# Optimization experiments

Measured on AMD Instinct MI355X. Metric: run time of the kernel, lower is better.

The kernel has to match this reference:

```python
import jax, jax.numpy as jnp
import numpy as np

N, D, H = 4096, 256, 8
DH = D // H
E = 131072
LN_EPS = 1e-5
NEG = -1e9


def setup_inputs() -> dict:
    key = jax.random.key(0)
    ks = jax.random.split(key, 10)
    s = 0.02
    return {
        "embeddings": jax.random.normal(ks[0], (N, D), dtype=jnp.float32),
        "edge_index": jax.random.randint(ks[1], (2, E), 0, N, dtype=jnp.int64),
        "in_proj_w": jax.random.normal(ks[2], (3 * D, D), dtype=jnp.float32) * s,
        "in_proj_b": jnp.zeros((3 * D,), jnp.float32),
        "out_w": jax.random.normal(ks[3], (D, D), dtype=jnp.float32) * s,
        "out_b": jnp.zeros((D,), jnp.float32),
        "lin_w": jax.random.normal(ks[4], (D, D), dtype=jnp.float32) * s,
        "lin_b": jnp.zeros((D,), jnp.float32),
        "ln_g": jnp.ones((D,), jnp.float32),
        "ln_beta": jnp.zeros((D,), jnp.float32),
    }


def reference(embeddings, edge_index, in_proj_w, in_proj_b, out_w, out_b, lin_w, lin_b, ln_g, ln_beta):
    n, d = embeddings.shape
    src, dst = edge_index[0], edge_index[1]
    # symmetric adjacency (per-cell neighbor set = unique nodes touching the cell),
    # self excluded (matches `neighbor_indices != cell_idx`)
    adj = jnp.zeros((n, n), dtype=bool).at[src, dst].set(True).at[dst, src].set(True)
    adj = adj & ~jnp.eye(n, dtype=bool)
    has_nb = adj.any(axis=1)  # [N]

    # MultiheadAttention (eval: dropout off), single query per cell over its neighbors
    qkv = embeddings @ in_proj_w.T + in_proj_b          # [N, 3D]
    q, k, v = jnp.split(qkv, 3, axis=-1)
    qh = q.reshape(n, H, DH)
    kh = k.reshape(n, H, DH)
    vh = v.reshape(n, H, DH)
    scale = 1.0 / np.sqrt(DH).astype(np.float32)
    scores = jnp.einsum('nhd,mhd->nhm', qh, kh) * scale  # [N, H, N]
    scores = jnp.where(adj[:, None, :], scores, NEG)
    attn = jax.nn.softmax(scores, axis=-1)
    ctx = jnp.einsum('nhm,mhd->nhd', attn, vh).reshape(n, d)
    ctx = ctx @ out_w.T + out_b
    # cells with no neighbors keep their own embedding
    x = jnp.where(has_nb[:, None], ctx, embeddings)

    # context_transform: Linear -> LayerNorm -> GELU (dropout off in eval)
    y = x @ lin_w.T + lin_b
    mu = y.mean(axis=-1, keepdims=True)
    var = y.var(axis=-1, keepdims=True)
    y = (y - mu) / jnp.sqrt(var + LN_EPS) * ln_g + ln_beta
    return jax.nn.gelu(y, approximate=False)
```

## Files before the change

kernel.cpp:

```cpp
#include <hip/hip_runtime.h>
#include <math.h>

#define NN 4096
#define DD 256
#define EE 131072
#define MAXD 128
#define SP 132

typedef __attribute__((ext_vector_type(8))) short short8;
typedef __attribute__((ext_vector_type(4))) float float4v;

__device__ __forceinline__ unsigned short f2bf(float f){
    unsigned u = __float_as_uint(f);
    return (unsigned short)((u + 0x7fffu + ((u >> 16) & 1u)) >> 16);
}
__device__ __forceinline__ float blo(unsigned u){ return __uint_as_float(u << 16); }
__device__ __forceinline__ float bhi(unsigned u){ return __uint_as_float(u & 0xffff0000u); }

__device__ __forceinline__ void pack_one(const float* __restrict__ src, unsigned short* __restrict__ dst, int e){
    int lane = e & 63;
    int row = ((e >> 9) << 4) + (lane & 15);
    int k0 = ((e >> 6) & 7) * 32 + ((lane >> 4) << 3);
    const float* p = src + row * DD + k0;
    short8 v;
    #pragma unroll
    for (int j = 0; j < 8; ++j) v[j] = (short)f2bf(p[j]);
    ((short8*)dst)[e] = v;
}

__global__ void k_packw(const float* __restrict__ ipw, const float* __restrict__ ow, const float* __restrict__ lw,
                        unsigned short* __restrict__ bipw, unsigned short* __restrict__ bow,
                        unsigned short* __restrict__ blw, unsigned* __restrict__ adj){
    int e = blockIdx.x * 256 + threadIdx.x;
    for (int i = e; i < 524288; i += 40960) adj[i] = 0u;
    if (e < 24576)       pack_one(ipw, bipw, e);
    else if (e < 32768)  pack_one(ow,  bow,  e - 24576);
    else                 pack_one(lw,  blw,  e - 32768);
}

__global__ void __launch_bounds__(256) k_gqkv(const float* __restrict__ emb, const unsigned short* __restrict__ Bp,
                                              const float* __restrict__ bias, float* __restrict__ qf,
                                              unsigned short* __restrict__ kb, unsigned short* __restrict__ vb,
                                              const int* __restrict__ ei, unsigned* __restrict__ adj){
    __shared__ float sA[16 * 260];
    int bx = blockIdx.x, by = blockIdx.y;
    int t = threadIdx.x, w = t >> 6, lane = t & 63;

    int gid = (by * gridDim.x + bx) * 256 + t;
    if (gid < EE){
        int s = ei[gid], d = ei[EE + gid];
        if (s != d){
            atomicOr(&adj[s * 128 + (d >> 5)], 1u << (d & 31));
            atomicOr(&adj[d * 128 + (s >> 5)], 1u << (s & 31));
        }
    }

    #pragma unroll
    for (int i = 0; i < 16; ++i)
        sA[i * 260 + t] = emb[(bx * 16 + i) * 256 + t];
    __syncthreads();

    int arow = lane & 15, ak0 = (lane >> 4) << 3;
    short8 af[8];
    #pragma unroll
    for (int s = 0; s < 8; ++s){
        const float* p = &sA[arow * 260 + s * 32 + ak0];
        #pragma unroll
        for (int j = 0; j < 8; ++j) af[s][j] = (short)f2bf(p[j]);
    }

    const short8* B8 = (const short8*)Bp;
    float4v acc[4];
    #pragma unroll
    for (int c = 0; c < 4; ++c) acc[c] = (float4v){0.f, 0.f, 0.f, 0.f};
    #pragma unroll
    for (int s = 0; s < 8; ++s){
        #pragma unroll
        for (int c = 0; c < 4; ++c){
            int to = by * 16 + w * 4 + c;
            acc[c] = __builtin_amdgcn_mfma_f32_16x16x32_bf16(af[s], B8[(to * 8 + s) * 64 + lane], acc[c], 0, 0, 0);
        }
    }
    int q = lane >> 4, col = lane & 15;
    #pragma unroll
    for (int c = 0; c < 4; ++c){
        int o = (w * 4 + c) * 16 + col;
        float bo = bias[by * 256 + o];
        #pragma unroll
        for (int r = 0; r < 4; ++r){
            int node = bx * 16 + q * 4 + r;
            float val = acc[c][r] + bo;
            if (by == 0)      qf[node * 256 + o] = val;
            else if (by == 1) kb[node * 256 + o] = f2bf(val);
            else              vb[node * 256 + o] = f2bf(val);
        }
    }
}

__device__ __forceinline__ float dot32(const float4* qa, uint4 a, uint4 b, uint4 c, uint4 d){
    float s;
    s  = qa[0].x*blo(a.x) + qa[0].y*bhi(a.x) + qa[0].z*blo(a.y) + qa[0].w*bhi(a.y);
    s += qa[1].x*blo(a.z) + qa[1].y*bhi(a.z) + qa[1].z*blo(a.w) + qa[1].w*bhi(a.w);
    s += qa[2].x*blo(b.x) + qa[2].y*bhi(b.x) + qa[2].z*blo(b.y) + qa[2].w*bhi(b.y);
    s += qa[3].x*blo(b.z) + qa[3].y*bhi(b.z) + qa[3].z*blo(b.w) + qa[3].w*bhi(b.w);
    s += qa[4].x*blo(c.x) + qa[4].y*bhi(c.x) + qa[4].z*blo(c.y) + qa[4].w*bhi(c.y);
    s += qa[5].x*blo(c.z) + qa[5].y*bhi(c.z) + qa[5].z*blo(c.w) + qa[5].w*bhi(c.w);
    s += qa[6].x*blo(d.x) + qa[6].y*bhi(d.x) + qa[6].z*blo(d.y) + qa[6].w*bhi(d.y);
    s += qa[7].x*blo(d.z) + qa[7].y*bhi(d.z) + qa[7].z*blo(d.w) + qa[7].w*bhi(d.w);
    return s;
}

__global__ void __launch_bounds__(512) k_attn_tail(
        const float* __restrict__ qf, const unsigned short* __restrict__ kb,
        const unsigned short* __restrict__ vb, const unsigned* __restrict__ adj,
        const float* __restrict__ emb,
        const unsigned short* __restrict__ Bow, const float* __restrict__ ob,
        const unsigned short* __restrict__ Blw, const float* __restrict__ lb,
        const float* __restrict__ g, const float* __restrict__ beta,
        float* __restrict__ out){
    __shared__ float  sS[8][8][SP];
    __shared__ int    sNbr[8][MAXD];
    __shared__ short8 sPk[512];
    __shared__ float  sInv[8][8];
    __shared__ int    sDeg[8];
    int bx = blockIdx.x, t = threadIdx.x;
    int wv = t >> 6, lane = t & 63;
    int n0 = bx * 8;
    int n = n0 + wv;
    float* xs = (float*)sS;

    uint2 aw = ((const uint2*)(adj + n * 128))[lane];
    int cnt = __popc(aw.x) + __popc(aw.y);
    int pre = cnt;
    #pragma unroll
    for (int off = 1; off < 64; off <<= 1){
        int tmp = __shfl_up(pre, off);
        if (lane >= off) pre += tmp;
    }
    int tot = __shfl(pre, 63);
    int dg = (tot < MAXD) ? tot : MAXD;
    if (lane == 63) sDeg[wv] = dg;
    int base = pre - cnt;
    int mb = lane * 64;
    unsigned b0 = aw.x, b1 = aw.y;
    while (b0){ int b = __ffs(b0) - 1; b0 &= b0 - 1u; if (base < MAXD) sNbr[wv][base] = mb + b; base++; }
    mb += 32;
    while (b1){ int b = __ffs(b1) - 1; b1 &= b1 - 1u; if (base < MAXD) sNbr[wv][base] = mb + b; base++; }

    if (dg > 0){
        asm volatile("s_waitcnt lgkmcnt(0)" ::: "memory");

        int js = lane >> 3, h = lane & 7;
        float4 qa[8];
        const float4* q4 = (const float4*)(qf + n * 256 + h * 32);
        #pragma unroll
        for (int i = 0; i < 8; ++i) qa[i] = q4[i];
        for (int jb = 0; jb < dg; jb += 16){
            int j0 = jb + js, j1 = jb + 8 + js;
            bool v0 = j0 < dg, v1 = j1 < dg;
            int m0 = v0 ? sNbr[wv][j0] : sNbr[wv][0];
            int m1 = v1 ? sNbr[wv][j1] : sNbr[wv][0];
            const uint4* kr0 = (const uint4*)(kb + m0 * 256) + h * 4;
            const uint4* kr1 = (const uint4*)(kb + m1 * 256) + h * 4;
            uint4 a0 = kr0[0], a1 = kr0[1], a2 = kr0[2], a3 = kr0[3];
            uint4 c0 = kr1[0], c1 = kr1[1], c2 = kr1[2], c3 = kr1[3];
            float s0 = dot32(qa, a0, a1, a2, a3) * 0.17677669529663687f;
            float s1 = dot32(qa, c0, c1, c2, c3) * 0.17677669529663687f;
            if (v0) sS[wv][h][j0] = s0;
            if (v1) sS[wv][h][j1] = s1;
        }
        asm volatile("s_waitcnt lgkmcnt(0)" ::: "memory");

        int h2 = lane >> 3, i2 = lane & 7;
        float m1 = -1e30f;
        for (int j = i2; j < dg; j += 8) m1 = fmaxf(m1, sS[wv][h2][j]);
        m1 = fmaxf(m1, __shfl_xor(m1, 1));
        m1 = fmaxf(m1, __shfl_xor(m1, 2));
        m1 = fmaxf(m1, __shfl_xor(m1, 4));
        float sum = 0.f;
        for (int j = i2; j < dg; j += 8){ float e = __expf(sS[wv][h2][j] - m1); sS[wv][h2][j] = e; sum += e; }
        sum += __shfl_xor(sum, 1);
        sum += __shfl_xor(sum, 2);
        sum += __shfl_xor(sum, 4);
        if (i2 == 0) sInv[wv][h2] = 1.0f / sum;
        asm volatile("s_waitcnt lgkmcnt(0)" ::: "memory");

        int h3 = lane >> 3;
        const uint2* vb2 = (const uint2*)vb;
        float4 O = {0.f, 0.f, 0.f, 0.f};
        int j = 0;
        for (; j + 8 <= dg; j += 8){
            uint2 uu[8]; float ww[8];
            #pragma unroll
            for (int k = 0; k < 8; ++k){
                uu[k] = vb2[sNbr[wv][j + k] * 64 + lane];
                ww[k] = sS[wv][h3][j + k];
            }
            #pragma unroll
            for (int k = 0; k < 8; ++k){
                O.x += ww[k] * blo(uu[k].x); O.y += ww[k] * bhi(uu[k].x);
                O.z += ww[k] * blo(uu[k].y); O.w += ww[k] * bhi(uu[k].y);
            }
        }
        for (; j < dg; ++j){
            uint2 u = vb2[sNbr[wv][j] * 64 + lane];
            float wgt = sS[wv][h3][j];
            O.x += wgt * blo(u.x); O.y += wgt * bhi(u.x);
            O.z += wgt * blo(u.y); O.w += wgt * bhi(u.y);
        }
        float inv = sInv[wv][h3];

        int d0 = lane * 4;
        int s  = d0 >> 5;
        int l2 = ((d0 >> 3) & 3) * 16 + wv;
        uint2 pk;
        pk.x = (unsigned)f2bf(O.x * inv) | ((unsigned)f2bf(O.y * inv) << 16);
        pk.y = (unsigned)f2bf(O.z * inv) | ((unsigned)f2bf(O.w * inv) << 16);
        ((uint2*)sPk)[(s * 64 + l2) * 2 + ((d0 & 7) >> 2)] = pk;
    }
    __syncthreads();

    const short8* B8 = (const short8*)Bow;
    float4v acc[2];
    #pragma unroll
    for (int c = 0; c < 2; ++c) acc[c] = (float4v){0.f, 0.f, 0.f, 0.f};
    #pragma unroll
    for (int s = 0; s < 8; ++s){
        short8 a = sPk[s * 64 + lane];
        #pragma unroll
        for (int c = 0; c < 2; ++c)
            acc[c] = __builtin_amdgcn_mfma_f32_16x16x32_bf16(a, B8[((wv * 2 + c) * 8 + s) * 64 + lane], acc[c], 0, 0, 0);
    }
    int q = lane >> 4, col = lane & 15;
    #pragma unroll
    for (int c = 0; c < 2; ++c){
        int o = (wv * 2 + c) * 16 + col;
        float bo = ob[o];
        #pragma unroll
        for (int r = 0; r < 4; ++r){
            int row = q * 4 + r;
            if (row < 8){
                float x = acc[c][r] + bo;
                if (sDeg[row] == 0) x = emb[(n0 + row) * 256 + o];
                xs[row * 264 + o] = x;
            }
        }
    }
    __syncthreads();

    {
        int l2 = t & 63, s = t >> 6;
        int mm = l2 & 15, k0 = s * 32 + ((l2 >> 4) << 3);
        short8 v;
        if (mm < 8){
            #pragma unroll
            for (int j = 0; j < 8; ++j) v[j] = (short)f2bf(xs[mm * 264 + k0 + j]);
        } else {
            #pragma unroll
            for (int j = 0; j < 8; ++j) v[j] = 0;
        }
        sPk[t] = v;
    }
    __syncthreads();

    const short8* B2 = (const short8*)Blw;
    float4v acc2[2];
    #pragma unroll
    for (int c = 0; c < 2; ++c) acc2[c] = (float4v){0.f, 0.f, 0.f, 0.f};
    #pragma unroll
    for (int s = 0; s < 8; ++s){
        short8 a = sPk[s * 64 + lane];
        #pragma unroll
        for (int c = 0; c < 2; ++c)
            acc2[c] = __builtin_amdgcn_mfma_f32_16x16x32_bf16(a, B2[((wv * 2 + c) * 8 + s) * 64 + lane], acc2[c], 0, 0, 0);
    }
    __syncthreads();
    #pragma unroll
    for (int c = 0; c < 2; ++c){
        int o = (wv * 2 + c) * 16 + col;
        float bo = lb[o];
        #pragma unroll
        for (int r = 0; r < 4; ++r){
            int row = q * 4 + r;
            if (row < 8) xs[row * 264 + o] = acc2[c][r] + bo;
        }
    }
    __syncthreads();

    int i = lane;
    float s1 = 0.f, s2 = 0.f;
    #pragma unroll
    for (int jj = 0; jj < 4; ++jj){ float v = xs[wv * 264 + i + 64 * jj]; s1 += v; s2 += v * v; }
    #pragma unroll
    for (int off = 32; off > 0; off >>= 1){ s1 += __shfl_xor(s1, off); s2 += __shfl_xor(s2, off); }
    float mu = s1 * (1.0f / 256.0f);
    float var = s2 * (1.0f / 256.0f) - mu * mu;
    float rs = rsqrtf(fmaxf(var, 0.f) + 1e-5f);
    int nbase = (n0 + wv) * 256;
    #pragma unroll
    for (int jj = 0; jj < 4; ++jj){
        int cc = i + 64 * jj;
        float z = (xs[wv * 264 + cc] - mu) * rs * g[cc] + beta[cc];
        out[nbase + cc] = 0.5f * z * (1.0f + erff(z * 0.70710678118654752f));
    }
}

extern "C" void kernel_launch(void* const* d_in, const int* in_sizes, int n_in,
                              void* d_out, int out_size, void* d_ws, size_t ws_size,
                              hipStream_t stream){
    const float* emb = (const float*)d_in[0];
    const int*   ei  = (const int*)d_in[1];
    const float* ipw = (const float*)d_in[2];
    const float* ipb = (const float*)d_in[3];
    const float* ow  = (const float*)d_in[4];
    const float* ob  = (const float*)d_in[5];
    const float* lw  = (const float*)d_in[6];
    const float* lb  = (const float*)d_in[7];
    const float* g   = (const float*)d_in[8];
    const float* bet = (const float*)d_in[9];

    char* ws = (char*)d_ws;
    unsigned*       adj  = (unsigned*)(ws);
    unsigned short* bipw = (unsigned short*)(ws + 2113536);
    unsigned short* bow  = (unsigned short*)(ws + 2506752);
    unsigned short* blw  = (unsigned short*)(ws + 2637824);
    float*          qf   = (float*)(ws + 2768896);
    unsigned short* kb   = (unsigned short*)(ws + 6963200);
    unsigned short* vb   = (unsigned short*)(ws + 9060352);

    k_packw    <<<160, 256, 0, stream>>>(ipw, ow, lw, bipw, bow, blw, adj);
    k_gqkv     <<<dim3(256, 3), 256, 0, stream>>>(emb, bipw, ipb, qf, kb, vb, ei, adj);
    k_attn_tail<<<512, 512, 0, stream>>>(qf, kb, vb, adj, emb, bow, ob, blw, lb, g, bet, (float*)d_out);
}
```

Baseline: 125.1 us.

## Split each node's attention across two waves, doubling block size to 1024

```diff
diff --git a/kernel.cpp b/kernel.cpp
--- a/kernel.cpp
+++ b/kernel.cpp
@@ -110,7 +110,7 @@
     return s;
 }
 
-__global__ void __launch_bounds__(512) k_attn_tail(
+__global__ void __launch_bounds__(1024, 8) k_attn_tail(
         const float* __restrict__ qf, const unsigned short* __restrict__ kb,
         const unsigned short* __restrict__ vb, const unsigned* __restrict__ adj,
         const float* __restrict__ emb,
@@ -119,14 +119,15 @@
         const float* __restrict__ g, const float* __restrict__ beta,
         float* __restrict__ out){
     __shared__ float  sS[8][8][SP];
-    __shared__ int    sNbr[8][MAXD];
+    __shared__ int    sNbr[16][MAXD];
     __shared__ short8 sPk[512];
     __shared__ float  sInv[8][8];
     __shared__ int    sDeg[8];
     int bx = blockIdx.x, t = threadIdx.x;
     int wv = t >> 6, lane = t & 63;
-    int n0 = bx * 8;
-    int n = n0 + wv;
+    int w = wv >> 1;
+    int p = wv & 1;
+    int n0 = bx * 8, n = n0 + w;
     float* xs = (float*)sS;
 
     uint2 aw = ((const uint2*)(adj + n * 128))[lane];
@@ -139,7 +140,7 @@
     }
     int tot = __shfl(pre, 63);
     int dg = (tot < MAXD) ? tot : MAXD;
-    if (lane == 63) sDeg[wv] = dg;
+    if (p == 0 && lane == 63) sDeg[w] = dg;
     int base = pre - cnt;
     int mb = lane * 64;
     unsigned b0 = aw.x, b1 = aw.y;
@@ -150,97 +151,93 @@
     if (dg > 0){
         asm volatile("s_waitcnt lgkmcnt(0)" ::: "memory");
 
-        int js = lane >> 3, h = lane & 7;
+        int js = lane >> 2, hl = lane & 3, ah = p * 4 + hl;
         float4 qa[8];
-        const float4* q4 = (const float4*)(qf + n * 256 + h * 32);
+        const float4* q4 = (const float4*)(qf + n * 256 + ah * 32);
         #pragma unroll
         for (int i = 0; i < 8; ++i) qa[i] = q4[i];
         for (int jb = 0; jb < dg; jb += 16){
-            int j0 = jb + js, j1 = jb + 8 + js;
-            bool v0 = j0 < dg, v1 = j1 < dg;
-            int m0 = v0 ? sNbr[wv][j0] : sNbr[wv][0];
-            int m1 = v1 ? sNbr[wv][j1] : sNbr[wv][0];
-            const uint4* kr0 = (const uint4*)(kb + m0 * 256) + h * 4;
-            const uint4* kr1 = (const uint4*)(kb + m1 * 256) + h * 4;
-            uint4 a0 = kr0[0], a1 = kr0[1], a2 = kr0[2], a3 = kr0[3];
-            uint4 c0 = kr1[0], c1 = kr1[1], c2 = kr1[2], c3 = kr1[3];
-            float s0 = dot32(qa, a0, a1, a2, a3) * 0.17677669529663687f;
-            float s1 = dot32(qa, c0, c1, c2, c3) * 0.17677669529663687f;
-            if (v0) sS[wv][h][j0] = s0;
-            if (v1) sS[wv][h][j1] = s1;
+            int j = jb + js;
+            bool v = j < dg;
+            int m = v ? sNbr[wv][j] : sNbr[wv][0];
+            const uint4* kr = (const uint4*)(kb + m * 256) + ah * 4;
+            uint4 a0 = kr[0], a1 = kr[1], a2 = kr[2], a3 = kr[3];
+            float s = dot32(qa, a0, a1, a2, a3) * 0.17677669529663687f;
+            if (v) sS[w][ah][j] = s;
         }
         asm volatile("s_waitcnt lgkmcnt(0)" ::: "memory");
 
-        int h2 = lane >> 3, i2 = lane & 7;
+        int i2 = lane >> 2;
         float m1 = -1e30f;
-        for (int j = i2; j < dg; j += 8) m1 = fmaxf(m1, sS[wv][h2][j]);
-        m1 = fmaxf(m1, __shfl_xor(m1, 1));
-        m1 = fmaxf(m1, __shfl_xor(m1, 2));
+        for (int j = i2; j < dg; j += 16) m1 = fmaxf(m1, sS[w][ah][j]);
         m1 = fmaxf(m1, __shfl_xor(m1, 4));
+        m1 = fmaxf(m1, __shfl_xor(m1, 8));
+        m1 = fmaxf(m1, __shfl_xor(m1, 16));
+        m1 = fmaxf(m1, __shfl_xor(m1, 32));
         float sum = 0.f;
-        for (int j = i2; j < dg; j += 8){ float e = __expf(sS[wv][h2][j] - m1); sS[wv][h2][j] = e; sum += e; }
-        sum += __shfl_xor(sum, 1);
-        sum += __shfl_xor(sum, 2);
+        for (int j = i2; j < dg; j += 16){ float e = __expf(sS[w][ah][j] - m1); sS[w][ah][j] = e; sum += e; }
         sum += __shfl_xor(sum, 4);
-        if (i2 == 0) sInv[wv][h2] = 1.0f / sum;
+        sum += __shfl_xor(sum, 8);
+        sum += __shfl_xor(sum, 16);
+        sum += __shfl_xor(sum, 32);
+        if (i2 == 0) sInv[w][ah] = 1.0f / sum;
         asm volatile("s_waitcnt lgkmcnt(0)" ::: "memory");
 
-        int h3 = lane >> 3;
+        int jp = lane >> 5, dq = lane & 31;
+        int d0 = p * 128 + dq * 4;
+        int ahv = d0 >> 5;
+        int vidx = d0 >> 2;
         const uint2* vb2 = (const uint2*)vb;
         float4 O = {0.f, 0.f, 0.f, 0.f};
-        int j = 0;
-        for (; j + 8 <= dg; j += 8){
-            uint2 uu[8]; float ww[8];
-            #pragma unroll
-            for (int k = 0; k < 8; ++k){
-                uu[k] = vb2[sNbr[wv][j + k] * 64 + lane];
-                ww[k] = sS[wv][h3][j + k];
-            }
-            #pragma unroll
-            for (int k = 0; k < 8; ++k){
-                O.x += ww[k] * blo(uu[k].x); O.y += ww[k] * bhi(uu[k].x);
-                O.z += ww[k] * blo(uu[k].y); O.w += ww[k] * bhi(uu[k].y);
-            }
-        }
-        for (; j < dg; ++j){
-            uint2 u = vb2[sNbr[wv][j] * 64 + lane];
-            float wgt = sS[wv][h3][j];
+        int j = jp;
+        for (; j + 6 < dg; j += 8){
+            int m0 = sNbr[wv][j], m1_ = sNbr[wv][j + 2], m2 = sNbr[wv][j + 4], m3 = sNbr[wv][j + 6];
+            uint2 u0 = vb2[m0 * 64 + vidx];
+            uint2 u1 = vb2[m1_ * 64 + vidx];
+            uint2 u2 = vb2[m2 * 64 + vidx];
+            uint2 u3 = vb2[m3 * 64 + vidx];
+            float w0 = sS[w][ahv][j], w1 = sS[w][ahv][j + 2], w2 = sS[w][ahv][j + 4], w3 = sS[w][ahv][j + 6];
+            O.x += w0 * blo(u0.x) + w1 * blo(u1.x) + w2 * blo(u2.x) + w3 * blo(u3.x);
+            O.y += w0 * bhi(u0.x) + w1 * bhi(u1.x) + w2 * bhi(u2.x) + w3 * bhi(u3.x);
+            O.z += w0 * blo(u0.y) + w1 * blo(u1.y) + w2 * blo(u2.y) + w3 * blo(u3.y);
+            O.w += w0 * bhi(u0.y) + w1 * bhi(u1.y) + w2 * bhi(u2.y) + w3 * bhi(u3.y);
+        }
+        for (; j < dg; j += 2){
+            uint2 u = vb2[sNbr[wv][j] * 64 + vidx];
+            float wgt = sS[w][ahv][j];
             O.x += wgt * blo(u.x); O.y += wgt * bhi(u.x);
             O.z += wgt * blo(u.y); O.w += wgt * bhi(u.y);
         }
-        float inv = sInv[wv][h3];
-
-        int d0 = lane * 4;
-        int s  = d0 >> 5;
-        int l2 = ((d0 >> 3) & 3) * 16 + wv;
-        uint2 pk;
-        pk.x = (unsigned)f2bf(O.x * inv) | ((unsigned)f2bf(O.y * inv) << 16);
-        pk.y = (unsigned)f2bf(O.z * inv) | ((unsigned)f2bf(O.w * inv) << 16);
-        ((uint2*)sPk)[(s * 64 + l2) * 2 + ((d0 & 7) >> 2)] = pk;
+        O.x += __shfl_xor(O.x, 32); O.y += __shfl_xor(O.y, 32);
+        O.z += __shfl_xor(O.z, 32); O.w += __shfl_xor(O.w, 32);
+        if (lane < 32){
+            float inv = sInv[w][ahv];
+            int s  = d0 >> 5;
+            int l2 = ((d0 >> 3) & 3) * 16 + w;
+            uint2 pk;
+            pk.x = (unsigned)f2bf(O.x * inv) | ((unsigned)f2bf(O.y * inv) << 16);
+            pk.y = (unsigned)f2bf(O.z * inv) | ((unsigned)f2bf(O.w * inv) << 16);
+            ((uint2*)sPk)[(s * 64 + l2) * 2 + ((d0 & 7) >> 2)] = pk;
+        }
     }
     __syncthreads();
 
     const short8* B8 = (const short8*)Bow;
-    float4v acc[2];
-    #pragma unroll
-    for (int c = 0; c < 2; ++c) acc[c] = (float4v){0.f, 0.f, 0.f, 0.f};
+    float4v acc = (float4v){0.f, 0.f, 0.f, 0.f};
     #pragma unroll
     for (int s = 0; s < 8; ++s){
         short8 a = sPk[s * 64 + lane];
-        #pragma unroll
-        for (int c = 0; c < 2; ++c)
-            acc[c] = __builtin_amdgcn_mfma_f32_16x16x32_bf16(a, B8[((wv * 2 + c) * 8 + s) * 64 + lane], acc[c], 0, 0, 0);
+        acc = __builtin_amdgcn_mfma_f32_16x16x32_bf16(a, B8[(wv * 8 + s) * 64 + lane], acc, 0, 0, 0);
     }
     int q = lane >> 4, col = lane & 15;
-    #pragma unroll
-    for (int c = 0; c < 2; ++c){
-        int o = (wv * 2 + c) * 16 + col;
+    {
+        int o = wv * 16 + col;
         float bo = ob[o];
         #pragma unroll
         for (int r = 0; r < 4; ++r){
             int row = q * 4 + r;
             if (row < 8){
-                float x = acc[c][r] + bo;
+                float x = acc[r] + bo;
                 if (sDeg[row] == 0) x = emb[(n0 + row) * 256 + o];
                 xs[row * 264 + o] = x;
             }
@@ -248,7 +245,7 @@
     }
     __syncthreads();
 
-    {
+    if (t < 512){
         int l2 = t & 63, s = t >> 6;
         int mm = l2 & 15, k0 = s * 32 + ((l2 >> 4) << 3);
         short8 v;
@@ -264,44 +261,41 @@
     __syncthreads();
 
     const short8* B2 = (const short8*)Blw;
-    float4v acc2[2];
-    #pragma unroll
-    for (int c = 0; c < 2; ++c) acc2[c] = (float4v){0.f, 0.f, 0.f, 0.f};
+    float4v acc2 = (float4v){0.f, 0.f, 0.f, 0.f};
     #pragma unroll
     for (int s = 0; s < 8; ++s){
         short8 a = sPk[s * 64 + lane];
-        #pragma unroll
-        for (int c = 0; c < 2; ++c)
-            acc2[c] = __builtin_amdgcn_mfma_f32_16x16x32_bf16(a, B2[((wv * 2 + c) * 8 + s) * 64 + lane], acc2[c], 0, 0, 0);
-    }
-    __syncthreads();
-    #pragma unroll
-    for (int c = 0; c < 2; ++c){
-        int o = (wv * 2 + c) * 16 + col;
+        acc2 = __builtin_amdgcn_mfma_f32_16x16x32_bf16(a, B2[(wv * 8 + s) * 64 + lane], acc2, 0, 0, 0);
+    }
+    __syncthreads();
+    {
+        int o = wv * 16 + col;
         float bo = lb[o];
         #pragma unroll
         for (int r = 0; r < 4; ++r){
             int row = q * 4 + r;
-            if (row < 8) xs[row * 264 + o] = acc2[c][r] + bo;
-        }
-    }
-    __syncthreads();
-
-    int i = lane;
-    float s1 = 0.f, s2 = 0.f;
-    #pragma unroll
-    for (int jj = 0; jj < 4; ++jj){ float v = xs[wv * 264 + i + 64 * jj]; s1 += v; s2 += v * v; }
-    #pragma unroll
-    for (int off = 32; off > 0; off >>= 1){ s1 += __shfl_xor(s1, off); s2 += __shfl_xor(s2, off); }
-    float mu = s1 * (1.0f / 256.0f);
-    float var = s2 * (1.0f / 256.0f) - mu * mu;
-    float rs = rsqrtf(fmaxf(var, 0.f) + 1e-5f);
-    int nbase = (n0 + wv) * 256;
-    #pragma unroll
-    for (int jj = 0; jj < 4; ++jj){
-        int cc = i + 64 * jj;
-        float z = (xs[wv * 264 + cc] - mu) * rs * g[cc] + beta[cc];
-        out[nbase + cc] = 0.5f * z * (1.0f + erff(z * 0.70710678118654752f));
+            if (row < 8) xs[row * 264 + o] = acc2[r] + bo;
+        }
+    }
+    __syncthreads();
+
+    if (wv < 8){
+        int i = lane;
+        float s1 = 0.f, s2 = 0.f;
+        #pragma unroll
+        for (int jj = 0; jj < 4; ++jj){ float v = xs[wv * 264 + i + 64 * jj]; s1 += v; s2 += v * v; }
+        #pragma unroll
+        for (int off = 32; off > 0; off >>= 1){ s1 += __shfl_xor(s1, off); s2 += __shfl_xor(s2, off); }
+        float mu = s1 * (1.0f / 256.0f);
+        float var = s2 * (1.0f / 256.0f) - mu * mu;
+        float rs = rsqrtf(fmaxf(var, 0.f) + 1e-5f);
+        int nbase = (n0 + wv) * 256;
+        #pragma unroll
+        for (int jj = 0; jj < 4; ++jj){
+            int cc = i + 64 * jj;
+            float z = (xs[wv * 264 + cc] - mu) * rs * g[cc] + beta[cc];
+            out[nbase + cc] = 0.5f * z * (1.0f + erff(z * 0.70710678118654752f));
+        }
     }
 }
 
@@ -330,5 +324,5 @@
 
     k_packw    <<<160, 256, 0, stream>>>(ipw, ow, lw, bipw, bow, blw, adj);
     k_gqkv     <<<dim3(256, 3), 256, 0, stream>>>(emb, bipw, ipb, qf, kb, vb, ei, adj);
-    k_attn_tail<<<512, 512, 0, stream>>>(qf, kb, vb, adj, emb, bow, ob, blw, lb, g, bet, (float*)d_out);
-}
+    k_attn_tail<<<512, 1024, 0, stream>>>(qf, kb, vb, adj, emb, bow, ob, blw, lb, g, bet, (float*)d_out);
+}
```

Result: slower. 129.3 us (+3.4%).

## Split each node's attention across two waves with merged partial softmax

Applied to the files above, without the earlier changes.

```diff
diff --git a/kernel.cpp b/kernel.cpp
--- a/kernel.cpp
+++ b/kernel.cpp
@@ -110,7 +110,7 @@
     return s;
 }
 
-__global__ void __launch_bounds__(512) k_attn_tail(
+__global__ void __launch_bounds__(512, 6) k_attn_tail(
         const float* __restrict__ qf, const unsigned short* __restrict__ kb,
         const unsigned short* __restrict__ vb, const unsigned* __restrict__ adj,
         const float* __restrict__ emb,
@@ -118,15 +118,17 @@
         const unsigned short* __restrict__ Blw, const float* __restrict__ lb,
         const float* __restrict__ g, const float* __restrict__ beta,
         float* __restrict__ out){
-    __shared__ float  sS[8][8][SP];
+    __shared__ float  sS[4][8][SP];
     __shared__ int    sNbr[8][MAXD];
     __shared__ short8 sPk[512];
-    __shared__ float  sInv[8][8];
-    __shared__ int    sDeg[8];
+    __shared__ float  sMax[4][8][2];
+    __shared__ float  sSum[4][8][2];
+    __shared__ float  sV[4][256];
+    __shared__ int    sDeg[4];
     int bx = blockIdx.x, t = threadIdx.x;
     int wv = t >> 6, lane = t & 63;
-    int n0 = bx * 8;
-    int n = n0 + wv;
+    int w = wv >> 1, par = wv & 1;
+    int n0 = bx * 4, n = n0 + w;
     float* xs = (float*)sS;
 
     uint2 aw = ((const uint2*)(adj + n * 128))[lane];
@@ -139,7 +141,7 @@
     }
     int tot = __shfl(pre, 63);
     int dg = (tot < MAXD) ? tot : MAXD;
-    if (lane == 63) sDeg[wv] = dg;
+    if (par == 0 && lane == 63) sDeg[w] = dg;
     int base = pre - cnt;
     int mb = lane * 64;
     unsigned b0 = aw.x, b1 = aw.y;
@@ -147,75 +149,78 @@
     mb += 32;
     while (b1){ int b = __ffs(b1) - 1; b1 &= b1 - 1u; if (base < MAXD) sNbr[wv][base] = mb + b; base++; }
 
+    int js = lane >> 3, h = lane & 7;
+    float m_par = -1e30f, l_par = 0.f;
     if (dg > 0){
         asm volatile("s_waitcnt lgkmcnt(0)" ::: "memory");
 
-        int js = lane >> 3, h = lane & 7;
         float4 qa[8];
         const float4* q4 = (const float4*)(qf + n * 256 + h * 32);
         #pragma unroll
         for (int i = 0; i < 8; ++i) qa[i] = q4[i];
-        for (int jb = 0; jb < dg; jb += 16){
-            int j0 = jb + js, j1 = jb + 8 + js;
-            bool v0 = j0 < dg, v1 = j1 < dg;
-            int m0 = v0 ? sNbr[wv][j0] : sNbr[wv][0];
-            int m1 = v1 ? sNbr[wv][j1] : sNbr[wv][0];
-            const uint4* kr0 = (const uint4*)(kb + m0 * 256) + h * 4;
-            const uint4* kr1 = (const uint4*)(kb + m1 * 256) + h * 4;
-            uint4 a0 = kr0[0], a1 = kr0[1], a2 = kr0[2], a3 = kr0[3];
-            uint4 c0 = kr1[0], c1 = kr1[1], c2 = kr1[2], c3 = kr1[3];
-            float s0 = dot32(qa, a0, a1, a2, a3) * 0.17677669529663687f;
-            float s1 = dot32(qa, c0, c1, c2, c3) * 0.17677669529663687f;
-            if (v0) sS[wv][h][j0] = s0;
-            if (v1) sS[wv][h][j1] = s1;
+        for (int j = 2 * js + par; j < dg; j += 16){
+            int m = sNbr[wv][j];
+            const uint4* kr = (const uint4*)(kb + m * 256) + h * 4;
+            uint4 a0 = kr[0], a1 = kr[1], a2 = kr[2], a3 = kr[3];
+            sS[w][h][j] = dot32(qa, a0, a1, a2, a3) * 0.17677669529663687f;
         }
         asm volatile("s_waitcnt lgkmcnt(0)" ::: "memory");
 
-        int h2 = lane >> 3, i2 = lane & 7;
-        float m1 = -1e30f;
-        for (int j = i2; j < dg; j += 8) m1 = fmaxf(m1, sS[wv][h2][j]);
-        m1 = fmaxf(m1, __shfl_xor(m1, 1));
-        m1 = fmaxf(m1, __shfl_xor(m1, 2));
-        m1 = fmaxf(m1, __shfl_xor(m1, 4));
-        float sum = 0.f;
-        for (int j = i2; j < dg; j += 8){ float e = __expf(sS[wv][h2][j] - m1); sS[wv][h2][j] = e; sum += e; }
-        sum += __shfl_xor(sum, 1);
-        sum += __shfl_xor(sum, 2);
-        sum += __shfl_xor(sum, 4);
-        if (i2 == 0) sInv[wv][h2] = 1.0f / sum;
+        for (int j = 2 * js + par; j < dg; j += 16) m_par = fmaxf(m_par, sS[w][h][j]);
+        m_par = fmaxf(m_par, __shfl_xor(m_par, 8));
+        m_par = fmaxf(m_par, __shfl_xor(m_par, 16));
+        m_par = fmaxf(m_par, __shfl_xor(m_par, 32));
+        for (int j = 2 * js + par; j < dg; j += 16) l_par += __expf(sS[w][h][j] - m_par);
+        l_par += __shfl_xor(l_par, 8);
+        l_par += __shfl_xor(l_par, 16);
+        l_par += __shfl_xor(l_par, 32);
+        if (js == 0){ sMax[w][h][par] = m_par; sSum[w][h][par] = l_par; }
+    }
+    __syncthreads();
+
+    float4 O = {0.f, 0.f, 0.f, 0.f};
+    if (dg > 0){
+        float m_o = sMax[w][h][1 - par], l_o = sSum[w][h][1 - par];
+        float gmax = fmaxf(m_par, m_o);
+        float gsum = l_par * __expf(m_par - gmax) + l_o * __expf(m_o - gmax);
+        float inv = 1.0f / gsum;
+        for (int j = 2 * js + par; j < dg; j += 16)
+            sS[w][h][j] = __expf(sS[w][h][j] - gmax) * inv;
         asm volatile("s_waitcnt lgkmcnt(0)" ::: "memory");
 
         int h3 = lane >> 3;
         const uint2* vb2 = (const uint2*)vb;
-        float4 O = {0.f, 0.f, 0.f, 0.f};
-        int j = 0;
-        for (; j + 8 <= dg; j += 8){
-            uint2 uu[8]; float ww[8];
-            #pragma unroll
-            for (int k = 0; k < 8; ++k){
-                uu[k] = vb2[sNbr[wv][j + k] * 64 + lane];
-                ww[k] = sS[wv][h3][j + k];
-            }
+        int j = par;
+        for (; j + 14 < dg; j += 16){
+            int mm[8]; float ww[8]; uint2 uu[8];
+            #pragma unroll
+            for (int k = 0; k < 8; ++k){ mm[k] = sNbr[wv][j + 2 * k]; ww[k] = sS[w][h3][j + 2 * k]; }
+            #pragma unroll
+            for (int k = 0; k < 8; ++k) uu[k] = vb2[mm[k] * 64 + lane];
             #pragma unroll
             for (int k = 0; k < 8; ++k){
                 O.x += ww[k] * blo(uu[k].x); O.y += ww[k] * bhi(uu[k].x);
                 O.z += ww[k] * blo(uu[k].y); O.w += ww[k] * bhi(uu[k].y);
             }
         }
-        for (; j < dg; ++j){
+        for (; j < dg; j += 2){
             uint2 u = vb2[sNbr[wv][j] * 64 + lane];
-            float wgt = sS[wv][h3][j];
+            float wgt = sS[w][h3][j];
             O.x += wgt * blo(u.x); O.y += wgt * bhi(u.x);
             O.z += wgt * blo(u.y); O.w += wgt * bhi(u.y);
         }
-        float inv = sInv[wv][h3];
-
+        if (par == 1) ((float4*)&sV[w][0])[lane] = O;
+    }
+    __syncthreads();
+    if (dg > 0 && par == 0){
+        float4 r = ((float4*)&sV[w][0])[lane];
+        O.x += r.x; O.y += r.y; O.z += r.z; O.w += r.w;
         int d0 = lane * 4;
         int s  = d0 >> 5;
-        int l2 = ((d0 >> 3) & 3) * 16 + wv;
+        int l2 = ((d0 >> 3) & 3) * 16 + w;
         uint2 pk;
-        pk.x = (unsigned)f2bf(O.x * inv) | ((unsigned)f2bf(O.y * inv) << 16);
-        pk.y = (unsigned)f2bf(O.z * inv) | ((unsigned)f2bf(O.w * inv) << 16);
+        pk.x = (unsigned)f2bf(O.x) | ((unsigned)f2bf(O.y) << 16);
+        pk.y = (unsigned)f2bf(O.z) | ((unsigned)f2bf(O.w) << 16);
         ((uint2*)sPk)[(s * 64 + l2) * 2 + ((d0 & 7) >> 2)] = pk;
     }
     __syncthreads();
@@ -239,10 +244,10 @@
         #pragma unroll
         for (int r = 0; r < 4; ++r){
             int row = q * 4 + r;
-            if (row < 8){
+            if (row < 4){
                 float x = acc[c][r] + bo;
                 if (sDeg[row] == 0) x = emb[(n0 + row) * 256 + o];
-                xs[row * 264 + o] = x;
+                xs[row * 257 + o] = x;
             }
         }
     }
@@ -252,12 +257,12 @@
         int l2 = t & 63, s = t >> 6;
         int mm = l2 & 15, k0 = s * 32 + ((l2 >> 4) << 3);
         short8 v;
-        if (mm < 8){
-            #pragma unroll
-            for (int j = 0; j < 8; ++j) v[j] = (short)f2bf(xs[mm * 264 + k0 + j]);
+        if (mm < 4){
+            #pragma unroll
+            for (int jj = 0; jj < 8; ++jj) v[jj] = (short)f2bf(xs[mm * 257 + k0 + jj]);
         } else {
             #pragma unroll
-            for (int j = 0; j < 8; ++j) v[j] = 0;
+            for (int jj = 0; jj < 8; ++jj) v[jj] = 0;
         }
         sPk[t] = v;
     }
@@ -274,7 +279,6 @@
         for (int c = 0; c < 2; ++c)
             acc2[c] = __builtin_amdgcn_mfma_f32_16x16x32_bf16(a, B2[((wv * 2 + c) * 8 + s) * 64 + lane], acc2[c], 0, 0, 0);
     }
-    __syncthreads();
     #pragma unroll
     for (int c = 0; c < 2; ++c){
         int o = (wv * 2 + c) * 16 + col;
@@ -282,26 +286,28 @@
         #pragma unroll
         for (int r = 0; r < 4; ++r){
             int row = q * 4 + r;
-            if (row < 8) xs[row * 264 + o] = acc2[c][r] + bo;
-        }
-    }
-    __syncthreads();
-
-    int i = lane;
-    float s1 = 0.f, s2 = 0.f;
-    #pragma unroll
-    for (int jj = 0; jj < 4; ++jj){ float v = xs[wv * 264 + i + 64 * jj]; s1 += v; s2 += v * v; }
-    #pragma unroll
-    for (int off = 32; off > 0; off >>= 1){ s1 += __shfl_xor(s1, off); s2 += __shfl_xor(s2, off); }
-    float mu = s1 * (1.0f / 256.0f);
-    float var = s2 * (1.0f / 256.0f) - mu * mu;
-    float rs = rsqrtf(fmaxf(var, 0.f) + 1e-5f);
-    int nbase = (n0 + wv) * 256;
-    #pragma unroll
-    for (int jj = 0; jj < 4; ++jj){
-        int cc = i + 64 * jj;
-        float z = (xs[wv * 264 + cc] - mu) * rs * g[cc] + beta[cc];
-        out[nbase + cc] = 0.5f * z * (1.0f + erff(z * 0.70710678118654752f));
+            if (row < 4) xs[row * 257 + o] = acc2[c][r] + bo;
+        }
+    }
+    __syncthreads();
+
+    if (wv < 4){
+        int i = lane;
+        float s1 = 0.f, s2 = 0.f;
+        #pragma unroll
+        for (int jj = 0; jj < 4; ++jj){ float v = xs[wv * 257 + i + 64 * jj]; s1 += v; s2 += v * v; }
+        #pragma unroll
+        for (int off = 32; off > 0; off >>= 1){ s1 += __shfl_xor(s1, off); s2 += __shfl_xor(s2, off); }
+        float mu = s1 * (1.0f / 256.0f);
+        float var = s2 * (1.0f / 256.0f) - mu * mu;
+        float rs = rsqrtf(fmaxf(var, 0.f) + 1e-5f);
+        int nbase = (n0 + wv) * 256;
+        #pragma unroll
+        for (int jj = 0; jj < 4; ++jj){
+            int cc = i + 64 * jj;
+            float z = (xs[wv * 257 + cc] - mu) * rs * g[cc] + beta[cc];
+            out[nbase + cc] = 0.5f * z * (1.0f + erff(z * 0.70710678118654752f));
+        }
     }
 }
 
@@ -330,5 +336,5 @@
 
     k_packw    <<<160, 256, 0, stream>>>(ipw, ow, lw, bipw, bow, blw, adj);
     k_gqkv     <<<dim3(256, 3), 256, 0, stream>>>(emb, bipw, ipb, qf, kb, vb, ei, adj);
-    k_attn_tail<<<512, 512, 0, stream>>>(qf, kb, vb, adj, emb, bow, ob, blw, lb, g, bet, (float*)d_out);
-}
+    k_attn_tail<<<1024, 512, 0, stream>>>(qf, kb, vb, adj, emb, bow, ob, blw, lb, g, bet, (float*)d_out);
+}
```

Measured after the change: 139.2 us. 11.3% more time.

## Enlarge QKV GEMM row tile, hoist Q load, widen V gather batches

Applied to the files above, without the earlier changes.

```diff
diff --git a/kernel.cpp b/kernel.cpp
--- a/kernel.cpp
+++ b/kernel.cpp
@@ -42,12 +42,11 @@
                                               const float* __restrict__ bias, float* __restrict__ qf,
                                               unsigned short* __restrict__ kb, unsigned short* __restrict__ vb,
                                               const int* __restrict__ ei, unsigned* __restrict__ adj){
-    __shared__ float sA[16 * 260];
+    __shared__ float sA[32 * 260];
     int bx = blockIdx.x, by = blockIdx.y;
     int t = threadIdx.x, w = t >> 6, lane = t & 63;
 
-    int gid = (by * gridDim.x + bx) * 256 + t;
-    if (gid < EE){
+    for (int gid = (by * 128 + bx) * 256 + t; gid < EE; gid += 98304){
         int s = ei[gid], d = ei[EE + gid];
         if (s != d){
             atomicOr(&adj[s * 128 + (d >> 5)], 1u << (d & 31));
@@ -56,30 +55,38 @@
     }
 
     #pragma unroll
-    for (int i = 0; i < 16; ++i)
-        sA[i * 260 + t] = emb[(bx * 16 + i) * 256 + t];
+    for (int i = 0; i < 32; ++i)
+        sA[i * 260 + t] = emb[(bx * 32 + i) * 256 + t];
     __syncthreads();
 
     int arow = lane & 15, ak0 = (lane >> 4) << 3;
-    short8 af[8];
+    short8 af[2][8];
+    #pragma unroll
+    for (int r = 0; r < 2; ++r)
+        #pragma unroll
+        for (int s = 0; s < 8; ++s){
+            const float* p = &sA[(r * 16 + arow) * 260 + s * 32 + ak0];
+            #pragma unroll
+            for (int j = 0; j < 8; ++j) af[r][s][j] = (short)f2bf(p[j]);
+        }
+
+    const short8* B8 = (const short8*)Bp;
+    float4v acc[2][4];
+    #pragma unroll
+    for (int r = 0; r < 2; ++r)
+        #pragma unroll
+        for (int c = 0; c < 4; ++c) acc[r][c] = (float4v){0.f, 0.f, 0.f, 0.f};
     #pragma unroll
     for (int s = 0; s < 8; ++s){
-        const float* p = &sA[arow * 260 + s * 32 + ak0];
-        #pragma unroll
-        for (int j = 0; j < 8; ++j) af[s][j] = (short)f2bf(p[j]);
-    }
-
-    const short8* B8 = (const short8*)Bp;
-    float4v acc[4];
-    #pragma unroll
-    for (int c = 0; c < 4; ++c) acc[c] = (float4v){0.f, 0.f, 0.f, 0.f};
-    #pragma unroll
-    for (int s = 0; s < 8; ++s){
-        #pragma unroll
-        for (int c = 0; c < 4; ++c){
-            int to = by * 16 + w * 4 + c;
-            acc[c] = __builtin_amdgcn_mfma_f32_16x16x32_bf16(af[s], B8[(to * 8 + s) * 64 + lane], acc[c], 0, 0, 0);
-        }
+        short8 bfr[4];
+        #pragma unroll
+        for (int c = 0; c < 4; ++c)
+            bfr[c] = B8[((by * 16 + w * 4 + c) * 8 + s) * 64 + lane];
+        #pragma unroll
+        for (int r = 0; r < 2; ++r)
+            #pragma unroll
+            for (int c = 0; c < 4; ++c)
+                acc[r][c] = __builtin_amdgcn_mfma_f32_16x16x32_bf16(af[r][s], bfr[c], acc[r][c], 0, 0, 0);
     }
     int q = lane >> 4, col = lane & 15;
     #pragma unroll
@@ -87,13 +94,15 @@
         int o = (w * 4 + c) * 16 + col;
         float bo = bias[by * 256 + o];
         #pragma unroll
-        for (int r = 0; r < 4; ++r){
-            int node = bx * 16 + q * 4 + r;
-            float val = acc[c][r] + bo;
-            if (by == 0)      qf[node * 256 + o] = val;
-            else if (by == 1) kb[node * 256 + o] = f2bf(val);
-            else              vb[node * 256 + o] = f2bf(val);
-        }
+        for (int r = 0; r < 2; ++r)
+            #pragma unroll
+            for (int rr = 0; rr < 4; ++rr){
+                int node = bx * 32 + r * 16 + q * 4 + rr;
+                float val = acc[r][c][rr] + bo;
+                if (by == 0)      qf[node * 256 + o] = val;
+                else if (by == 1) kb[node * 256 + o] = f2bf(val);
+                else              vb[node * 256 + o] = f2bf(val);
+            }
     }
 }
 
@@ -129,6 +138,14 @@
     int n = n0 + wv;
     float* xs = (float*)sS;
 
+    int h = lane & 7;
+    float4 qa[8];
+    {
+        const float4* q4 = (const float4*)(qf + n * 256 + h * 32);
+        #pragma unroll
+        for (int i = 0; i < 8; ++i) qa[i] = q4[i];
+    }
+
     uint2 aw = ((const uint2*)(adj + n * 128))[lane];
     int cnt = __popc(aw.x) + __popc(aw.y);
     int pre = cnt;
@@ -150,11 +167,7 @@
     if (dg > 0){
         asm volatile("s_waitcnt lgkmcnt(0)" ::: "memory");
 
-        int js = lane >> 3, h = lane & 7;
-        float4 qa[8];
-        const float4* q4 = (const float4*)(qf + n * 256 + h * 32);
-        #pragma unroll
-        for (int i = 0; i < 8; ++i) qa[i] = q4[i];
+        int js = lane >> 3;
         for (int jb = 0; jb < dg; jb += 16){
             int j0 = jb + js, j1 = jb + 8 + js;
             bool v0 = j0 < dg, v1 = j1 < dg;
@@ -188,25 +201,21 @@
         int h3 = lane >> 3;
         const uint2* vb2 = (const uint2*)vb;
         float4 O = {0.f, 0.f, 0.f, 0.f};
-        int j = 0;
-        for (; j + 8 <= dg; j += 8){
-            uint2 uu[8]; float ww[8];
-            #pragma unroll
-            for (int k = 0; k < 8; ++k){
-                uu[k] = vb2[sNbr[wv][j + k] * 64 + lane];
-                ww[k] = sS[wv][h3][j + k];
+        for (int jb = 0; jb < dg; jb += 16){
+            uint2 uu[16]; float ww[16];
+            #pragma unroll
+            for (int k = 0; k < 16; ++k){
+                int j = jb + k;
+                bool v = j < dg;
+                int m = v ? sNbr[wv][j] : sNbr[wv][0];
+                ww[k] = v ? sS[wv][h3][j] : 0.f;
+                uu[k] = vb2[m * 64 + lane];
             }
             #pragma unroll
-            for (int k = 0; k < 8; ++k){
+            for (int k = 0; k < 16; ++k){
                 O.x += ww[k] * blo(uu[k].x); O.y += ww[k] * bhi(uu[k].x);
                 O.z += ww[k] * blo(uu[k].y); O.w += ww[k] * bhi(uu[k].y);
             }
-        }
-        for (; j < dg; ++j){
-            uint2 u = vb2[sNbr[wv][j] * 64 + lane];
-            float wgt = sS[wv][h3][j];
-            O.x += wgt * blo(u.x); O.y += wgt * bhi(u.x);
-            O.z += wgt * blo(u.y); O.w += wgt * bhi(u.y);
         }
         float inv = sInv[wv][h3];
 
@@ -287,21 +296,23 @@
     }
     __syncthreads();
 
-    int i = lane;
-    float s1 = 0.f, s2 = 0.f;
-    #pragma unroll
-    for (int jj = 0; jj < 4; ++jj){ float v = xs[wv * 264 + i + 64 * jj]; s1 += v; s2 += v * v; }
-    #pragma unroll
-    for (int off = 32; off > 0; off >>= 1){ s1 += __shfl_xor(s1, off); s2 += __shfl_xor(s2, off); }
-    float mu = s1 * (1.0f / 256.0f);
-    float var = s2 * (1.0f / 256.0f) - mu * mu;
-    float rs = rsqrtf(fmaxf(var, 0.f) + 1e-5f);
-    int nbase = (n0 + wv) * 256;
-    #pragma unroll
-    for (int jj = 0; jj < 4; ++jj){
-        int cc = i + 64 * jj;
-        float z = (xs[wv * 264 + cc] - mu) * rs * g[cc] + beta[cc];
-        out[nbase + cc] = 0.5f * z * (1.0f + erff(z * 0.70710678118654752f));
+    {
+        int i = lane;
+        float s1 = 0.f, s2 = 0.f;
+        #pragma unroll
+        for (int jj = 0; jj < 4; ++jj){ float v = xs[wv * 264 + i + 64 * jj]; s1 += v; s2 += v * v; }
+        #pragma unroll
+        for (int off = 32; off > 0; off >>= 1){ s1 += __shfl_xor(s1, off); s2 += __shfl_xor(s2, off); }
+        float mu = s1 * (1.0f / 256.0f);
+        float var = s2 * (1.0f / 256.0f) - mu * mu;
+        float rs = rsqrtf(fmaxf(var, 0.f) + 1e-5f);
+        int nbase = (n0 + wv) * 256;
+        #pragma unroll
+        for (int jj = 0; jj < 4; ++jj){
+            int cc = i + 64 * jj;
+            float z = (xs[wv * 264 + cc] - mu) * rs * g[cc] + beta[cc];
+            out[nbase + cc] = 0.5f * z * (1.0f + erff(z * 0.70710678118654752f));
+        }
     }
 }
 
@@ -329,6 +340,6 @@
     unsigned short* vb   = (unsigned short*)(ws + 9060352);
 
     k_packw    <<<160, 256, 0, stream>>>(ipw, ow, lw, bipw, bow, blw, adj);
-    k_gqkv     <<<dim3(256, 3), 256, 0, stream>>>(emb, bipw, ipb, qf, kb, vb, ei, adj);
+    k_gqkv     <<<dim3(128, 3), 256, 0, stream>>>(emb, bipw, ipb, qf, kb, vb, ei, adj);
     k_attn_tail<<<512, 512, 0, stream>>>(qf, kb, vb, adj, emb, bow, ob, blw, lb, g, bet, (float*)d_out);
 }
```

Measured after the change: 127.2 us. About the same (+1.7%).
